# Kernel optimization log

Hardware: AMD Instinct MI355X
Metric: run time of the kernel (lower is better)

## Reference

```python
import jax, jax.numpy as jnp
import numpy as np

EPS = 1e-6
GROUPS = 32


def group_norm(x, scale, bias):
    # x: [b, c, d, h, w]
    b, c, d, h, w = x.shape
    xg = x.reshape(b, GROUPS, c // GROUPS, d, h, w)
    mean = xg.mean(axis=(2, 3, 4, 5), keepdims=True)
    var = xg.var(axis=(2, 3, 4, 5), keepdims=True)
    xn = ((xg - mean) * jax.lax.rsqrt(var + EPS)).reshape(b, c, d, h, w)
    return xn * scale[None, :, None, None, None] + bias[None, :, None, None, None]


def setup_inputs() -> dict:
    key = jax.random.key(0)
    ks = jax.random.split(key, 6)
    C = 512
    x = jax.random.normal(ks[0], (2, C, 16, 16, 16), dtype=jnp.float32)
    s = 1.0 / np.sqrt(C)
    return {
        "x": x,
        "gn_scale": jnp.ones((C,), jnp.float32),
        "gn_bias": jnp.zeros((C,), jnp.float32),
        "wq": jax.random.normal(ks[1], (C, C), jnp.float32) * s,
        "bq": jnp.zeros((C,), jnp.float32),
        "wk": jax.random.normal(ks[2], (C, C), jnp.float32) * s,
        "bk": jnp.zeros((C,), jnp.float32),
        "wv": jax.random.normal(ks[3], (C, C), jnp.float32) * s,
        "bv": jnp.zeros((C,), jnp.float32),
        "wproj": jax.random.normal(ks[4], (C, C), jnp.float32) * s,
        "bproj": jnp.zeros((C,), jnp.float32),
    }


def reference(x, gn_scale, gn_bias, wq, bq, wk, bk, wv, bv, wproj, bproj):
    b, c, d, h, w = x.shape
    h_ = group_norm(x, gn_scale, gn_bias)
    hf = h_.reshape(b, c, d * h * w)  # [b, c, N]
    # 1x1x1 convs == per-position channel matmuls
    q = jnp.einsum("oc,bcn->bon", wq, hf) + bq[None, :, None]
    k = jnp.einsum("oc,bcn->bon", wk, hf) + bk[None, :, None]
    v = jnp.einsum("oc,bcn->bon", wv, hf) + bv[None, :, None]
    # attn[b, i, j] = softmax_j(q_i . k_j / sqrt(c))
    attn = jnp.einsum("bci,bcj->bij", q, k) * (c ** -0.5)
    attn = jax.nn.softmax(attn, axis=-1)
    # out[b, c, i] = sum_j v[b, c, j] * attn[b, i, j]
    out = jnp.einsum("bcj,bij->bci", v, attn)
    out = jnp.einsum("oc,bcn->bon", wproj, out) + bproj[None, :, None]
    return x + out.reshape(b, c, d, h, w)
```

## Files before the change

### kernel.cpp

```cpp
#include <hip/hip_runtime.h>
#include <hip/hip_bf16.h>

#define BB 2
#define CC 512
#define GG 32
#define NN 4096
#define EPSV 1e-6f

typedef __attribute__((ext_vector_type(4))) float f32x4;
typedef __attribute__((ext_vector_type(8))) short s16x8;
typedef __attribute__((ext_vector_type(4))) short s16x4;

__device__ __forceinline__ ushort f2bf(float f){
  union { float f; unsigned u; } v; v.f = f;
  unsigned r = v.u + 0x7fffu + ((v.u >> 16) & 1u);
  return (ushort)(r >> 16);
}
__device__ __forceinline__ short f2bfs(float f){ return (short)f2bf(f); }
__device__ __forceinline__ float b2f(ushort u){
  union { unsigned u; float f; } v; v.u = ((unsigned)u) << 16; return v.f;
}

__device__ __forceinline__ f32x4 mfma16(s16x8 a, s16x8 b, f32x4 c){
  return __builtin_amdgcn_mfma_f32_16x16x32_bf16(a, b, c, 0, 0, 0);
}

#define GLOAD_LDS16(g, l) __builtin_amdgcn_global_load_lds( \
    (const __attribute__((address_space(1))) void*)(g),     \
    (__attribute__((address_space(3))) void*)(l), 16, 0, 0)

__global__ __launch_bounds__(256) void k_convert_w(const float* __restrict__ wq, const float* __restrict__ wk,
                                                   const float* __restrict__ wv, const float* __restrict__ wp,
                                                   ushort* __restrict__ wbf){
  int idx = blockIdx.x * 256 + threadIdx.x;
  const float* srcs[4] = {wq, wk, wv, wp};
  #pragma unroll
  for (int m = 0; m < 4; m++){
    float4 v = reinterpret_cast<const float4*>(srcs[m])[idx];
    ushort4 o; o.x = f2bf(v.x); o.y = f2bf(v.y); o.z = f2bf(v.z); o.w = f2bf(v.w);
    reinterpret_cast<ushort4*>(wbf + (size_t)m * CC * CC)[idx] = o;
  }
}

__global__ __launch_bounds__(256) void k_gn_stats(const float* __restrict__ x, float* __restrict__ stats){
  int bg = blockIdx.x;
  const float* p = x + (size_t)bg * (16 * NN);
  float s = 0.f, ss = 0.f;
  for (int i = threadIdx.x; i < 16 * NN / 4; i += 256){
    float4 v = reinterpret_cast<const float4*>(p)[i];
    s  += v.x + v.y + v.z + v.w;
    ss += v.x*v.x + v.y*v.y + v.z*v.z + v.w*v.w;
  }
  #pragma unroll
  for (int off = 32; off; off >>= 1){ s += __shfl_down(s, off); ss += __shfl_down(ss, off); }
  __shared__ float rs_[4], rss_[4];
  int w = threadIdx.x >> 6, lane = threadIdx.x & 63;
  if (lane == 0){ rs_[w] = s; rss_[w] = ss; }
  __syncthreads();
  if (threadIdx.x == 0){
    float S = rs_[0] + rs_[1] + rs_[2] + rs_[3];
    float SS = rss_[0] + rss_[1] + rss_[2] + rss_[3];
    float inv = 1.0f / (16.0f * NN);
    float mean = S * inv;
    float var = SS * inv - mean * mean;
    stats[bg * 2 + 0] = mean;
    stats[bg * 2 + 1] = rsqrtf(var + EPSV);
  }
}

__global__ __launch_bounds__(256) void k_gn_apply(const float* __restrict__ x, const float* __restrict__ gsc,
                                                  const float* __restrict__ gbi, const float* __restrict__ stats,
                                                  ushort* __restrict__ hf){
  __shared__ ushort tr[32][520];
  int b = blockIdx.y;
  int nb = blockIdx.x * 32;
  int t = threadIdx.x;
  int n = t & 31, cr = t >> 5;
  const float* xb = x + (size_t)b * CC * NN;
  for (int c0 = 0; c0 < CC; c0 += 8){
    int c = c0 + cr;
    float mean = stats[(b * GG + (c >> 4)) * 2 + 0];
    float rstd = stats[(b * GG + (c >> 4)) * 2 + 1];
    float v = xb[(size_t)c * NN + nb + n];
    tr[n][c] = f2bf((v - mean) * rstd * gsc[c] + gbi[c]);
  }
  __syncthreads();
  ushort* out = hf + ((size_t)b * NN + nb) * CC;
  int c8 = (t & 63) * 8;
  int nrow0 = t >> 6;
  #pragma unroll
  for (int i = 0; i < 8; i++){
    int nr = nrow0 + i * 4;
    *reinterpret_cast<s16x8*>(&out[(size_t)nr * CC + c8]) =
      *reinterpret_cast<const s16x8*>(&tr[nr][c8]);
  }
}

__global__ __launch_bounds__(256) void k_gemm_qkv(const ushort* __restrict__ W, const ushort* __restrict__ Bt,
                                                  const float* __restrict__ bq, const float* __restrict__ bk,
                                                  const float* __restrict__ bv,
                                                  ushort* __restrict__ qo, ushort* __restrict__ ko,
                                                  ushort* __restrict__ vo, float rs){
  __shared__ ushort Al[3][64][72];
  __shared__ ushort Bl[64][72];
  __shared__ float bl[3][64];
  int b = blockIdx.z, ob = blockIdx.y * 64, nb = blockIdx.x * 64;
  int t = threadIdx.x, w = t >> 6, l = t & 63;
  int lr = l & 15, lk = l >> 4;
  int wo = (w >> 1) * 32, wn = (w & 1) * 32;
  if (t < 64){ bl[0][t] = bq[ob + t]; bl[1][t] = bk[ob + t]; bl[2][t] = bv[ob + t]; }
  const ushort* Bp = Bt + ((size_t)b * NN + nb) * CC;
  int srow = t >> 2, scol = (t & 3) * 16;
  f32x4 acc[3][2][2] = {};
  for (int k0 = 0; k0 < CC; k0 += 64){
    #pragma unroll
    for (int m = 0; m < 3; m++){
      const ushort* Ap = W + (size_t)m * CC * CC + (size_t)ob * CC;
      *reinterpret_cast<s16x8*>(&Al[m][srow][scol])     = *reinterpret_cast<const s16x8*>(&Ap[(size_t)srow * CC + k0 + scol]);
      *reinterpret_cast<s16x8*>(&Al[m][srow][scol + 8]) = *reinterpret_cast<const s16x8*>(&Ap[(size_t)srow * CC + k0 + scol + 8]);
    }
    *reinterpret_cast<s16x8*>(&Bl[srow][scol])     = *reinterpret_cast<const s16x8*>(&Bp[(size_t)srow * CC + k0 + scol]);
    *reinterpret_cast<s16x8*>(&Bl[srow][scol + 8]) = *reinterpret_cast<const s16x8*>(&Bp[(size_t)srow * CC + k0 + scol + 8]);
    __syncthreads();
    #pragma unroll
    for (int kk = 0; kk < 2; kk++){
      s16x8 b0 = *reinterpret_cast<const s16x8*>(&Bl[wn + lr][kk * 32 + lk * 8]);
      s16x8 b1 = *reinterpret_cast<const s16x8*>(&Bl[wn + 16 + lr][kk * 32 + lk * 8]);
      #pragma unroll
      for (int m = 0; m < 3; m++){
        s16x8 a0 = *reinterpret_cast<const s16x8*>(&Al[m][wo + lr][kk * 32 + lk * 8]);
        s16x8 a1 = *reinterpret_cast<const s16x8*>(&Al[m][wo + 16 + lr][kk * 32 + lk * 8]);
        acc[m][0][0] = mfma16(a0, b0, acc[m][0][0]);
        acc[m][0][1] = mfma16(a0, b1, acc[m][0][1]);
        acc[m][1][0] = mfma16(a1, b0, acc[m][1][0]);
        acc[m][1][1] = mfma16(a1, b1, acc[m][1][1]);
      }
    }
    __syncthreads();
  }
  #pragma unroll
  for (int m = 0; m < 2; m++){
    ushort* dst = (m == 0) ? qo : ko;
    float scl = (m == 0) ? rs : 1.0f;
    #pragma unroll
    for (int oi = 0; oi < 2; oi++)
      #pragma unroll
      for (int nj = 0; nj < 2; nj++){
        int o0 = wo + oi * 16 + lk * 4;
        int n  = nb + wn + nj * 16 + lr;
        s16x4 pv;
        #pragma unroll
        for (int r = 0; r < 4; r++) pv[r] = f2bfs((acc[m][oi][nj][r] + bl[m][o0 + r]) * scl);
        *reinterpret_cast<s16x4*>(&dst[((size_t)b * NN + n) * CC + ob + o0]) = pv;
      }
  }
  #pragma unroll
  for (int oi = 0; oi < 2; oi++)
    #pragma unroll
    for (int nj = 0; nj < 2; nj++){
      int o0 = wo + oi * 16 + lk * 4;
      int ncl = wn + nj * 16 + lr;
      #pragma unroll
      for (int r = 0; r < 4; r++) Al[0][o0 + r][ncl] = f2bf(acc[2][oi][nj][r] + bl[2][o0 + r]);
    }
  __syncthreads();
  {
    int o = t >> 2, ns = (t & 3) * 16;
    ushort* dst = &vo[((size_t)b * CC + ob + o) * NN + nb + ns];
    *reinterpret_cast<s16x8*>(dst)     = *reinterpret_cast<const s16x8*>(&Al[0][o][ns]);
    *reinterpret_cast<s16x8*>(dst + 8) = *reinterpret_cast<const s16x8*>(&Al[0][o][ns + 8]);
  }
}

__global__ __launch_bounds__(256) void k_gemm_s(const ushort* __restrict__ qt, const ushort* __restrict__ kt,
                                                ushort* __restrict__ P, float* __restrict__ part){
  __shared__ __align__(16) char smem[65536];
  int lin = blockIdx.x + 32 * blockIdx.y + 1024 * blockIdx.z;
  int tt0 = (lin & 7) * 256 + (lin >> 3);
  int jblk = tt0 & 31;
  int pair = tt0 >> 5;
  int b = pair >> 5;
  int j0 = jblk * 128, i0 = (pair & 31) * 128;
  int t = threadIdx.x, w = t >> 6, l = t & 63;
  int lr = l & 15, lk = l >> 4;
  int wj = (w >> 1) * 64, wi = (w & 1) * 64;
  const ushort* kb = kt + ((size_t)b * NN + j0) * CC;
  const ushort* qb = qt + ((size_t)b * NN + i0) * CC;
  int srow = l >> 3;
  int schunk = (l & 7) ^ srow;

#define STAGE_S(BUF, K0)                                                          \
  {                                                                               \
    ushort* Ks_ = (ushort*)(smem + (BUF) * 16384);                                \
    ushort* Qs_ = (ushort*)(smem + 32768 + (BUF) * 16384);                        \
    _Pragma("unroll")                                                             \
    for (int tt = 0; tt < 8; tt++){                                               \
      int inst = w * 8 + tt;                                                      \
      if (inst < 16){                                                             \
        const ushort* src = kb + (size_t)(inst * 8 + srow) * CC + (K0) + schunk * 8; \
        GLOAD_LDS16(src, Ks_ + inst * 512);                                       \
      } else {                                                                    \
        int q = inst - 16;                                                        \
        const ushort* src = qb + (size_t)(q * 8 + srow) * CC + (K0) + schunk * 8; \
        GLOAD_LDS16(src, Qs_ + q * 512);                                          \
      }                                                                           \
    }                                                                             \
  }

  f32x4 acc[4][4] = {};
  STAGE_S(0, 0)
  __syncthreads();
  for (int s8 = 0; s8 < 8; s8++){
    if (s8 < 7) STAGE_S((s8 + 1) & 1, (s8 + 1) * 64)
    const ushort* Ks = (const ushort*)(smem + (s8 & 1) * 16384);
    const ushort* Qs = (const ushort*)(smem + 32768 + (s8 & 1) * 16384);
    #pragma unroll
    for (int kk = 0; kk < 2; kk++){
      int xs = ((kk * 4 + lk) ^ (lr & 7)) * 8;
      s16x8 af[4], bf[4];
      #pragma unroll
      for (int s = 0; s < 4; s++){
        af[s] = *(const s16x8*)&Ks[(wj + s * 16 + lr) * 64 + xs];
        bf[s] = *(const s16x8*)&Qs[(wi + s * 16 + lr) * 64 + xs];
      }
      #pragma unroll
      for (int sj = 0; sj < 4; sj++)
        #pragma unroll
        for (int si = 0; si < 4; si++)
          acc[sj][si] = mfma16(af[sj], bf[si], acc[sj][si]);
    }
    __syncthreads();
  }
#undef STAGE_S
  ushort* Pe = (ushort*)smem;
  float rsum[4] = {0.f, 0.f, 0.f, 0.f};
  #pragma unroll
  for (int sj = 0; sj < 4; sj++)
    #pragma unroll
    for (int si = 0; si < 4; si++){
      int il = wi + si * 16 + lr;
      int jl = wj + sj * 16 + lk * 4;
      s16x4 pk;
      #pragma unroll
      for (int r = 0; r < 4; r++){
        float e = exp2f(acc[sj][si][r]);
        pk[r] = f2bfs(e);
        rsum[si] += e;
      }
      *(s16x4*)&Pe[il * 136 + jl] = pk;
    }
  #pragma unroll
  for (int si = 0; si < 4; si++){
    float s = rsum[si];
    s += __shfl_xor(s, 16);
    s += __shfl_xor(s, 32);
    if (lk == 0){
      int il = wi + si * 16 + lr;
      part[((size_t)b * NN + i0 + il) * 64 + jblk * 2 + (w >> 1)] = s;
    }
  }
  __syncthreads();
  {
    int row = t >> 1, cs = (t & 1) * 64;
    ushort* dst = P + ((size_t)b * NN + i0 + row) * NN + j0 + cs;
    #pragma unroll
    for (int k = 0; k < 8; k++)
      *(s16x8*)&dst[k * 8] = *(const s16x8*)&Pe[row * 136 + cs + k * 8];
  }
}

__global__ __launch_bounds__(256) void k_rowsum2(const float* __restrict__ part, float* __restrict__ linv){
  int row = blockIdx.x * 4 + (threadIdx.x >> 6);
  int l = threadIdx.x & 63;
  float s = part[(size_t)row * 64 + l];
  #pragma unroll
  for (int off = 32; off; off >>= 1) s += __shfl_down(s, off);
  if (l == 0) linv[row] = 1.0f / s;
}

__global__ __launch_bounds__(512) void k_gemm_o(const ushort* __restrict__ P, const ushort* __restrict__ vv,
                                                const float* __restrict__ linv, ushort* __restrict__ ot){
  __shared__ __align__(16) char smem[49152];
  int lin = blockIdx.x + 8 * blockIdx.y + 256 * blockIdx.z;
  int tt0 = (lin & 7) * 64 + (lin >> 3);
  int cblk = tt0 & 7;
  int pair = tt0 >> 3;
  int b = pair >> 5;
  int c0 = cblk * 64, i0 = (pair & 31) * 128;
  int t = threadIdx.x, w = t >> 6, l = t & 63;
  int lr = l & 15, lk = l >> 4;
  int wi = (w >> 1) * 32, wc = (w & 1) * 32;
  const ushort* vb = vv + ((size_t)b * CC + c0) * NN;
  const ushort* pb = P + ((size_t)b * NN + i0) * NN;
  int srow = l >> 3;
  int schunk = (l & 7) ^ srow;

#define STAGE_O(BUF, K0)                                                          \
  {                                                                               \
    ushort* Vs_ = (ushort*)(smem + (BUF) * 8192);                                 \
    ushort* Ps_ = (ushort*)(smem + 16384 + (BUF) * 16384);                        \
    _Pragma("unroll")                                                             \
    for (int tt = 0; tt < 3; tt++){                                               \
      int inst = w * 3 + tt;                                                      \
      if (inst < 8){                                                              \
        const ushort* src = vb + (size_t)(inst * 8 + srow) * NN + (K0) + schunk * 8; \
        GLOAD_LDS16(src, Vs_ + inst * 512);                                       \
      } else {                                                                    \
        int q = inst - 8;                                                         \
        const ushort* src = pb + (size_t)(q * 8 + srow) * NN + (K0) + schunk * 8; \
        GLOAD_LDS16(src, Ps_ + q * 512);                                          \
      }                                                                           \
    }                                                                             \
  }

  f32x4 acc[2][2] = {};
  STAGE_O(0, 0)
  __syncthreads();
  for (int s64 = 0; s64 < 64; s64++){
    if (s64 < 63) STAGE_O((s64 + 1) & 1, (s64 + 1) * 64)
    const ushort* Vs = (const ushort*)(smem + (s64 & 1) * 8192);
    const ushort* Ps = (const ushort*)(smem + 16384 + (s64 & 1) * 16384);
    #pragma unroll
    for (int kk = 0; kk < 2; kk++){
      int xs = ((kk * 4 + lk) ^ (lr & 7)) * 8;
      s16x8 af[2], bf[2];
      af[0] = *(const s16x8*)&Vs[(wc + lr) * 64 + xs];
      af[1] = *(const s16x8*)&Vs[(wc + 16 + lr) * 64 + xs];
      bf[0] = *(const s16x8*)&Ps[(wi + lr) * 64 + xs];
      bf[1] = *(const s16x8*)&Ps[(wi + 16 + lr) * 64 + xs];
      acc[0][0] = mfma16(af[0], bf[0], acc[0][0]);
      acc[0][1] = mfma16(af[0], bf[1], acc[0][1]);
      acc[1][0] = mfma16(af[1], bf[0], acc[1][0]);
      acc[1][1] = mfma16(af[1], bf[1], acc[1][1]);
    }
    __syncthreads();
  }
#undef STAGE_O
  ushort* Oe = (ushort*)smem;
  #pragma unroll
  for (int si = 0; si < 2; si++){
    int il = wi + si * 16 + lr;
    float li = linv[(size_t)b * NN + i0 + il];
    #pragma unroll
    for (int sc = 0; sc < 2; sc++){
      int cl = wc + sc * 16 + lk * 4;
      s16x4 pk;
      #pragma unroll
      for (int r = 0; r < 4; r++) pk[r] = f2bfs(acc[sc][si][r] * li);
      *(s16x4*)&Oe[il * 72 + cl] = pk;
    }
  }
  __syncthreads();
  {
    int row = t >> 2, cs = (t & 3) * 16;
    ushort* dst = ot + ((size_t)b * NN + i0 + row) * CC + c0 + cs;
    #pragma unroll
    for (int k = 0; k < 2; k++)
      *(s16x8*)&dst[k * 8] = *(const s16x8*)&Oe[row * 72 + cs + k * 8];
  }
}

__global__ __launch_bounds__(256) void k_gemm_proj(const ushort* __restrict__ A, const ushort* __restrict__ Bt,
                                                   const float* __restrict__ bias, float* __restrict__ o32,
                                                   const float* __restrict__ xres){
  __shared__ ushort Al[64][72];
  __shared__ ushort Bl[64][72];
  __shared__ float bl[64];
  __shared__ float trf[64 * 68];
  int b = blockIdx.z, ob = blockIdx.y * 64, nb = blockIdx.x * 64;
  int t = threadIdx.x, w = t >> 6, l = t & 63;
  int lr = l & 15, lk = l >> 4;
  int wo = (w >> 1) * 32, wn = (w & 1) * 32;
  if (t < 64) bl[t] = bias[ob + t];
  const ushort* Bp = Bt + ((size_t)b * NN + nb) * CC;
  const ushort* Ap = A + (size_t)ob * CC;
  int srow = t >> 2, scol = (t & 3) * 16;
  f32x4 acc[2][2] = {};
  for (int k0 = 0; k0 < CC; k0 += 64){
    *reinterpret_cast<s16x8*>(&Al[srow][scol])     = *reinterpret_cast<const s16x8*>(&Ap[(size_t)srow * CC + k0 + scol]);
    *reinterpret_cast<s16x8*>(&Al[srow][scol + 8]) = *reinterpret_cast<const s16x8*>(&Ap[(size_t)srow * CC + k0 + scol + 8]);
    *reinterpret_cast<s16x8*>(&Bl[srow][scol])     = *reinterpret_cast<const s16x8*>(&Bp[(size_t)srow * CC + k0 + scol]);
    *reinterpret_cast<s16x8*>(&Bl[srow][scol + 8]) = *reinterpret_cast<const s16x8*>(&Bp[(size_t)srow * CC + k0 + scol + 8]);
    __syncthreads();
    #pragma unroll
    for (int kk = 0; kk < 2; kk++){
      s16x8 a0 = *reinterpret_cast<const s16x8*>(&Al[wo + lr][kk * 32 + lk * 8]);
      s16x8 a1 = *reinterpret_cast<const s16x8*>(&Al[wo + 16 + lr][kk * 32 + lk * 8]);
      s16x8 b0 = *reinterpret_cast<const s16x8*>(&Bl[wn + lr][kk * 32 + lk * 8]);
      s16x8 b1 = *reinterpret_cast<const s16x8*>(&Bl[wn + 16 + lr][kk * 32 + lk * 8]);
      acc[0][0] = mfma16(a0, b0, acc[0][0]);
      acc[0][1] = mfma16(a0, b1, acc[0][1]);
      acc[1][0] = mfma16(a1, b0, acc[1][0]);
      acc[1][1] = mfma16(a1, b1, acc[1][1]);
    }
    __syncthreads();
  }
  #pragma unroll
  for (int oi = 0; oi < 2; oi++)
    #pragma unroll
    for (int nj = 0; nj < 2; nj++){
      int o0 = wo + oi * 16 + lk * 4;
      int ncl = wn + nj * 16 + lr;
      #pragma unroll
      for (int r = 0; r < 4; r++) trf[(o0 + r) * 68 + ncl] = acc[oi][nj][r] + bl[o0 + r];
    }
  __syncthreads();
  {
    int o = t >> 2, ns = (t & 3) * 16;
    size_t base = ((size_t)b * CC + ob + o) * NN + nb + ns;
    #pragma unroll
    for (int q = 0; q < 4; q++){
      float4 xv = *reinterpret_cast<const float4*>(&xres[base + q * 4]);
      float4 ov;
      ov.x = xv.x + trf[o * 68 + ns + q * 4 + 0];
      ov.y = xv.y + trf[o * 68 + ns + q * 4 + 1];
      ov.z = xv.z + trf[o * 68 + ns + q * 4 + 2];
      ov.w = xv.w + trf[o * 68 + ns + q * 4 + 3];
      *reinterpret_cast<float4*>(&o32[base + q * 4]) = ov;
    }
  }
}

extern "C" void kernel_launch(void* const* d_in, const int* in_sizes, int n_in,
                              void* d_out, int out_size, void* d_ws, size_t ws_size,
                              hipStream_t stream){
  const float* x   = (const float*)d_in[0];
  const float* gsc = (const float*)d_in[1];
  const float* gbi = (const float*)d_in[2];
  const float* wq  = (const float*)d_in[3];
  const float* bq  = (const float*)d_in[4];
  const float* wk  = (const float*)d_in[5];
  const float* bk  = (const float*)d_in[6];
  const float* wv  = (const float*)d_in[7];
  const float* bv  = (const float*)d_in[8];
  const float* wp  = (const float*)d_in[9];
  const float* bp  = (const float*)d_in[10];
  char* ws = (char*)d_ws;
  const size_t MB = 1024 * 1024;
  ushort* wbf  = (ushort*)ws;
  ushort* qtb  = (ushort*)(ws + 2 * MB);
  ushort* ktb  = (ushort*)(ws + 10 * MB);
  ushort* vvb  = (ushort*)(ws + 18 * MB);
  ushort* hfb  = (ushort*)(ws + 26 * MB);
  ushort* Pbuf = (ushort*)(ws + 34 * MB);
  float* linv  = (float*)(ws + 98 * MB);
  float* stats = (float*)(ws + 98 * MB + 64 * 1024);
  float* part  = (float*)(ws + 26 * MB);
  ushort* otb = hfb;

  const float rs = 0.044194173824159216f * 1.4426950408889634f;

  k_convert_w<<<256, 256, 0, stream>>>(wq, wk, wv, wp, wbf);
  k_gn_stats<<<64, 256, 0, stream>>>(x, stats);
  k_gn_apply<<<dim3(128, 2, 1), 256, 0, stream>>>(x, gsc, gbi, stats, hfb);
  k_gemm_qkv<<<dim3(64, 8, 2), 256, 0, stream>>>(wbf, hfb, bq, bk, bv, qtb, ktb, vvb, rs);
  k_gemm_s<<<dim3(32, 32, 2), 256, 0, stream>>>(qtb, ktb, Pbuf, part);
  k_rowsum2<<<2048, 256, 0, stream>>>(part, linv);
  k_gemm_o<<<dim3(8, 32, 2), 512, 0, stream>>>(Pbuf, vvb, linv, otb);
  k_gemm_proj<<<dim3(64, 8, 2), 256, 0, stream>>>(wbf + 3 * CC * CC, otb, bp, (float*)d_out, x);
}
```

Measured before the change: 194.0 us.

## Double-buffer QKV/proj GEMMs with async LDS loads and shrink S-GEMM k-step

```diff
diff --git a/kernel.cpp b/kernel.cpp
--- a/kernel.cpp
+++ b/kernel.cpp
@@ -96,85 +96,106 @@
   }
 }
 
-__global__ __launch_bounds__(256) void k_gemm_qkv(const ushort* __restrict__ W, const ushort* __restrict__ Bt,
-                                                  const float* __restrict__ bq, const float* __restrict__ bk,
-                                                  const float* __restrict__ bv,
-                                                  ushort* __restrict__ qo, ushort* __restrict__ ko,
-                                                  ushort* __restrict__ vo, float rs){
-  __shared__ ushort Al[3][64][72];
-  __shared__ ushort Bl[64][72];
+__global__ __launch_bounds__(256, 3) void k_gemm_qkv2(const ushort* __restrict__ W, const ushort* __restrict__ Bt,
+                                                      const float* __restrict__ bq, const float* __restrict__ bk,
+                                                      const float* __restrict__ bv,
+                                                      ushort* __restrict__ qo, ushort* __restrict__ ko,
+                                                      ushort* __restrict__ vo, float rs){
+  __shared__ __align__(16) char smem[40960];
   __shared__ float bl[3][64];
-  int b = blockIdx.z, ob = blockIdx.y * 64, nb = blockIdx.x * 64;
+  int b = blockIdx.z, ob = blockIdx.y * 64, nb = blockIdx.x * 128;
   int t = threadIdx.x, w = t >> 6, l = t & 63;
   int lr = l & 15, lk = l >> 4;
-  int wo = (w >> 1) * 32, wn = (w & 1) * 32;
+  int wo = (w >> 1) * 32, wn = (w & 1) * 64;
   if (t < 64){ bl[0][t] = bq[ob + t]; bl[1][t] = bk[ob + t]; bl[2][t] = bv[ob + t]; }
   const ushort* Bp = Bt + ((size_t)b * NN + nb) * CC;
-  int srow = t >> 2, scol = (t & 3) * 16;
-  f32x4 acc[3][2][2] = {};
-  for (int k0 = 0; k0 < CC; k0 += 64){
+  const ushort* Wp = W + (size_t)ob * CC;
+  int srow = l >> 2;
+  int schunk = (l & 3) ^ ((l >> 2) & 3) ^ ((l >> 4) & 3);
+  int xs = (lk ^ (lr & 3) ^ ((lr >> 2) & 3)) * 8;
+
+#define STAGE_QKV(BUF, K0)                                                               \
+  {                                                                                      \
+    ushort* As_ = (ushort*)(smem + (BUF) * 20480);                                       \
+    ushort* Bs_ = As_ + 6144;                                                            \
+    _Pragma("unroll")                                                                    \
+    for (int tt = 0; tt < 5; tt++){                                                      \
+      int inst = w * 5 + tt;                                                             \
+      if (inst < 12){                                                                    \
+        int m = inst >> 2, sub = inst & 3;                                               \
+        const ushort* src = Wp + (size_t)m * CC * CC + (size_t)(sub * 16 + srow) * CC + (K0) + schunk * 8; \
+        GLOAD_LDS16(src, As_ + m * 2048 + sub * 512);                                    \
+      } else {                                                                           \
+        int q = inst - 12;                                                               \
+        const ushort* src = Bp + (size_t)(q * 16 + srow) * CC + (K0) + schunk * 8;       \
+        GLOAD_LDS16(src, Bs_ + q * 512);                                                 \
+      }                                                                                  \
+    }                                                                                    \
+  }
+
+  f32x4 acc[3][2][4] = {};
+  STAGE_QKV(0, 0)
+  __syncthreads();
+  for (int s16 = 0; s16 < 16; s16++){
+    if (s16 < 15) STAGE_QKV((s16 + 1) & 1, (s16 + 1) * 32)
+    const ushort* As = (const ushort*)(smem + (s16 & 1) * 20480);
+    const ushort* Bs = As + 6144;
+    s16x8 bf[4];
+    #pragma unroll
+    for (int sn = 0; sn < 4; sn++)
+      bf[sn] = *(const s16x8*)&Bs[(wn + sn * 16 + lr) * 32 + xs];
     #pragma unroll
     for (int m = 0; m < 3; m++){
-      const ushort* Ap = W + (size_t)m * CC * CC + (size_t)ob * CC;
-      *reinterpret_cast<s16x8*>(&Al[m][srow][scol])     = *reinterpret_cast<const s16x8*>(&Ap[(size_t)srow * CC + k0 + scol]);
-      *reinterpret_cast<s16x8*>(&Al[m][srow][scol + 8]) = *reinterpret_cast<const s16x8*>(&Ap[(size_t)srow * CC + k0 + scol + 8]);
-    }
-    *reinterpret_cast<s16x8*>(&Bl[srow][scol])     = *reinterpret_cast<const s16x8*>(&Bp[(size_t)srow * CC + k0 + scol]);
-    *reinterpret_cast<s16x8*>(&Bl[srow][scol + 8]) = *reinterpret_cast<const s16x8*>(&Bp[(size_t)srow * CC + k0 + scol + 8]);
+      s16x8 a0 = *(const s16x8*)&As[m * 2048 + (wo + lr) * 32 + xs];
+      s16x8 a1 = *(const s16x8*)&As[m * 2048 + (wo + 16 + lr) * 32 + xs];
+      #pragma unroll
+      for (int sn = 0; sn < 4; sn++){
+        acc[m][0][sn] = mfma16(a0, bf[sn], acc[m][0][sn]);
+        acc[m][1][sn] = mfma16(a1, bf[sn], acc[m][1][sn]);
+      }
+    }
     __syncthreads();
-    #pragma unroll
-    for (int kk = 0; kk < 2; kk++){
-      s16x8 b0 = *reinterpret_cast<const s16x8*>(&Bl[wn + lr][kk * 32 + lk * 8]);
-      s16x8 b1 = *reinterpret_cast<const s16x8*>(&Bl[wn + 16 + lr][kk * 32 + lk * 8]);
-      #pragma unroll
-      for (int m = 0; m < 3; m++){
-        s16x8 a0 = *reinterpret_cast<const s16x8*>(&Al[m][wo + lr][kk * 32 + lk * 8]);
-        s16x8 a1 = *reinterpret_cast<const s16x8*>(&Al[m][wo + 16 + lr][kk * 32 + lk * 8]);
-        acc[m][0][0] = mfma16(a0, b0, acc[m][0][0]);
-        acc[m][0][1] = mfma16(a0, b1, acc[m][0][1]);
-        acc[m][1][0] = mfma16(a1, b0, acc[m][1][0]);
-        acc[m][1][1] = mfma16(a1, b1, acc[m][1][1]);
-      }
-    }
-    __syncthreads();
-  }
+  }
+#undef STAGE_QKV
   #pragma unroll
   for (int m = 0; m < 2; m++){
     ushort* dst = (m == 0) ? qo : ko;
     float scl = (m == 0) ? rs : 1.0f;
     #pragma unroll
-    for (int oi = 0; oi < 2; oi++)
-      #pragma unroll
-      for (int nj = 0; nj < 2; nj++){
-        int o0 = wo + oi * 16 + lk * 4;
-        int n  = nb + wn + nj * 16 + lr;
+    for (int so = 0; so < 2; so++)
+      #pragma unroll
+      for (int sn = 0; sn < 4; sn++){
+        int o0 = wo + so * 16 + lk * 4;
+        int n  = nb + wn + sn * 16 + lr;
         s16x4 pv;
         #pragma unroll
-        for (int r = 0; r < 4; r++) pv[r] = f2bfs((acc[m][oi][nj][r] + bl[m][o0 + r]) * scl);
+        for (int r = 0; r < 4; r++) pv[r] = f2bfs((acc[m][so][sn][r] + bl[m][o0 + r]) * scl);
         *reinterpret_cast<s16x4*>(&dst[((size_t)b * NN + n) * CC + ob + o0]) = pv;
       }
   }
-  #pragma unroll
-  for (int oi = 0; oi < 2; oi++)
-    #pragma unroll
-    for (int nj = 0; nj < 2; nj++){
-      int o0 = wo + oi * 16 + lk * 4;
-      int ncl = wn + nj * 16 + lr;
-      #pragma unroll
-      for (int r = 0; r < 4; r++) Al[0][o0 + r][ncl] = f2bf(acc[2][oi][nj][r] + bl[2][o0 + r]);
+  ushort* Ve = (ushort*)smem;
+  #pragma unroll
+  for (int so = 0; so < 2; so++)
+    #pragma unroll
+    for (int sn = 0; sn < 4; sn++){
+      int o0 = wo + so * 16 + lk * 4;
+      int ncl = wn + sn * 16 + lr;
+      #pragma unroll
+      for (int r = 0; r < 4; r++) Ve[(o0 + r) * 136 + ncl] = f2bf(acc[2][so][sn][r] + bl[2][o0 + r]);
     }
   __syncthreads();
   {
-    int o = t >> 2, ns = (t & 3) * 16;
-    ushort* dst = &vo[((size_t)b * CC + ob + o) * NN + nb + ns];
-    *reinterpret_cast<s16x8*>(dst)     = *reinterpret_cast<const s16x8*>(&Al[0][o][ns]);
-    *reinterpret_cast<s16x8*>(dst + 8) = *reinterpret_cast<const s16x8*>(&Al[0][o][ns + 8]);
-  }
-}
-
-__global__ __launch_bounds__(256) void k_gemm_s(const ushort* __restrict__ qt, const ushort* __restrict__ kt,
-                                                ushort* __restrict__ P, float* __restrict__ part){
-  __shared__ __align__(16) char smem[65536];
+    int row = t >> 2, cs = (t & 3) * 32;
+    ushort* dst = &vo[((size_t)b * CC + ob + row) * NN + nb + cs];
+    #pragma unroll
+    for (int k = 0; k < 4; k++)
+      *(s16x8*)&dst[k * 8] = *(const s16x8*)&Ve[row * 136 + cs + k * 8];
+  }
+}
+
+__global__ __launch_bounds__(256, 4) void k_gemm_s(const ushort* __restrict__ qt, const ushort* __restrict__ kt,
+                                                   ushort* __restrict__ P, float* __restrict__ part){
+  __shared__ __align__(16) char smem[35840];
   int lin = blockIdx.x + 32 * blockIdx.y + 1024 * blockIdx.z;
   int tt0 = (lin & 7) * 256 + (lin >> 3);
   int jblk = tt0 & 31;
@@ -186,22 +207,23 @@
   int wj = (w >> 1) * 64, wi = (w & 1) * 64;
   const ushort* kb = kt + ((size_t)b * NN + j0) * CC;
   const ushort* qb = qt + ((size_t)b * NN + i0) * CC;
-  int srow = l >> 3;
-  int schunk = (l & 7) ^ srow;
+  int srow = l >> 2;
+  int schunk = (l & 3) ^ ((l >> 2) & 3) ^ ((l >> 4) & 3);
+  int xs = (lk ^ (lr & 3) ^ ((lr >> 2) & 3)) * 8;
 
 #define STAGE_S(BUF, K0)                                                          \
   {                                                                               \
-    ushort* Ks_ = (ushort*)(smem + (BUF) * 16384);                                \
-    ushort* Qs_ = (ushort*)(smem + 32768 + (BUF) * 16384);                        \
+    ushort* Ks_ = (ushort*)(smem + (BUF) * 8192);                                 \
+    ushort* Qs_ = (ushort*)(smem + 16384 + (BUF) * 8192);                         \
     _Pragma("unroll")                                                             \
-    for (int tt = 0; tt < 8; tt++){                                               \
-      int inst = w * 8 + tt;                                                      \
-      if (inst < 16){                                                             \
-        const ushort* src = kb + (size_t)(inst * 8 + srow) * CC + (K0) + schunk * 8; \
+    for (int tt = 0; tt < 4; tt++){                                               \
+      int inst = w * 4 + tt;                                                      \
+      if (inst < 8){                                                              \
+        const ushort* src = kb + (size_t)(inst * 16 + srow) * CC + (K0) + schunk * 8; \
         GLOAD_LDS16(src, Ks_ + inst * 512);                                       \
       } else {                                                                    \
-        int q = inst - 16;                                                        \
-        const ushort* src = qb + (size_t)(q * 8 + srow) * CC + (K0) + schunk * 8; \
+        int q = inst - 8;                                                         \
+        const ushort* src = qb + (size_t)(q * 16 + srow) * CC + (K0) + schunk * 8; \
         GLOAD_LDS16(src, Qs_ + q * 512);                                          \
       }                                                                           \
     }                                                                             \
@@ -210,25 +232,21 @@
   f32x4 acc[4][4] = {};
   STAGE_S(0, 0)
   __syncthreads();
-  for (int s8 = 0; s8 < 8; s8++){
-    if (s8 < 7) STAGE_S((s8 + 1) & 1, (s8 + 1) * 64)
-    const ushort* Ks = (const ushort*)(smem + (s8 & 1) * 16384);
-    const ushort* Qs = (const ushort*)(smem + 32768 + (s8 & 1) * 16384);
-    #pragma unroll
-    for (int kk = 0; kk < 2; kk++){
-      int xs = ((kk * 4 + lk) ^ (lr & 7)) * 8;
-      s16x8 af[4], bf[4];
-      #pragma unroll
-      for (int s = 0; s < 4; s++){
-        af[s] = *(const s16x8*)&Ks[(wj + s * 16 + lr) * 64 + xs];
-        bf[s] = *(const s16x8*)&Qs[(wi + s * 16 + lr) * 64 + xs];
-      }
-      #pragma unroll
-      for (int sj = 0; sj < 4; sj++)
-        #pragma unroll
-        for (int si = 0; si < 4; si++)
-          acc[sj][si] = mfma16(af[sj], bf[si], acc[sj][si]);
-    }
+  for (int s8 = 0; s8 < 16; s8++){
+    if (s8 < 15) STAGE_S((s8 + 1) & 1, (s8 + 1) * 32)
+    const ushort* Ks = (const ushort*)(smem + (s8 & 1) * 8192);
+    const ushort* Qs = (const ushort*)(smem + 16384 + (s8 & 1) * 8192);
+    s16x8 af[4], bf[4];
+    #pragma unroll
+    for (int s = 0; s < 4; s++){
+      af[s] = *(const s16x8*)&Ks[(wj + s * 16 + lr) * 32 + xs];
+      bf[s] = *(const s16x8*)&Qs[(wi + s * 16 + lr) * 32 + xs];
+    }
+    #pragma unroll
+    for (int sj = 0; sj < 4; sj++)
+      #pragma unroll
+      for (int si = 0; si < 4; si++)
+        acc[sj][si] = mfma16(af[sj], bf[si], acc[sj][si]);
     __syncthreads();
   }
 #undef STAGE_S
@@ -360,62 +378,80 @@
   }
 }
 
-__global__ __launch_bounds__(256) void k_gemm_proj(const ushort* __restrict__ A, const ushort* __restrict__ Bt,
-                                                   const float* __restrict__ bias, float* __restrict__ o32,
-                                                   const float* __restrict__ xres){
-  __shared__ ushort Al[64][72];
-  __shared__ ushort Bl[64][72];
+__global__ __launch_bounds__(256, 3) void k_gemm_proj2(const ushort* __restrict__ A, const ushort* __restrict__ Bt,
+                                                       const float* __restrict__ bias, float* __restrict__ o32,
+                                                       const float* __restrict__ xres){
+  __shared__ __align__(16) char smem[34048];
   __shared__ float bl[64];
-  __shared__ float trf[64 * 68];
-  int b = blockIdx.z, ob = blockIdx.y * 64, nb = blockIdx.x * 64;
+  int b = blockIdx.z, ob = blockIdx.y * 64, nb = blockIdx.x * 128;
   int t = threadIdx.x, w = t >> 6, l = t & 63;
   int lr = l & 15, lk = l >> 4;
-  int wo = (w >> 1) * 32, wn = (w & 1) * 32;
+  int wo = (w >> 1) * 32, wn = (w & 1) * 64;
   if (t < 64) bl[t] = bias[ob + t];
   const ushort* Bp = Bt + ((size_t)b * NN + nb) * CC;
   const ushort* Ap = A + (size_t)ob * CC;
-  int srow = t >> 2, scol = (t & 3) * 16;
-  f32x4 acc[2][2] = {};
-  for (int k0 = 0; k0 < CC; k0 += 64){
-    *reinterpret_cast<s16x8*>(&Al[srow][scol])     = *reinterpret_cast<const s16x8*>(&Ap[(size_t)srow * CC + k0 + scol]);
-    *reinterpret_cast<s16x8*>(&Al[srow][scol + 8]) = *reinterpret_cast<const s16x8*>(&Ap[(size_t)srow * CC + k0 + scol + 8]);
-    *reinterpret_cast<s16x8*>(&Bl[srow][scol])     = *reinterpret_cast<const s16x8*>(&Bp[(size_t)srow * CC + k0 + scol]);
-    *reinterpret_cast<s16x8*>(&Bl[srow][scol + 8]) = *reinterpret_cast<const s16x8*>(&Bp[(size_t)srow * CC + k0 + scol + 8]);
+  int srow = l >> 2;
+  int schunk = (l & 3) ^ ((l >> 2) & 3) ^ ((l >> 4) & 3);
+  int xs = (lk ^ (lr & 3) ^ ((lr >> 2) & 3)) * 8;
+
+#define STAGE_P2(BUF, K0)                                                         \
+  {                                                                               \
+    ushort* As_ = (ushort*)(smem + (BUF) * 12288);                                \
+    ushort* Bs_ = As_ + 2048;                                                     \
+    _Pragma("unroll")                                                             \
+    for (int tt = 0; tt < 3; tt++){                                               \
+      int inst = w * 3 + tt;                                                      \
+      if (inst < 4){                                                              \
+        const ushort* src = Ap + (size_t)(inst * 16 + srow) * CC + (K0) + schunk * 8; \
+        GLOAD_LDS16(src, As_ + inst * 512);                                       \
+      } else {                                                                    \
+        int q = inst - 4;                                                         \
+        const ushort* src = Bp + (size_t)(q * 16 + srow) * CC + (K0) + schunk * 8; \
+        GLOAD_LDS16(src, Bs_ + q * 512);                                          \
+      }                                                                           \
+    }                                                                             \
+  }
+
+  f32x4 acc[2][4] = {};
+  STAGE_P2(0, 0)
+  __syncthreads();
+  for (int s16 = 0; s16 < 16; s16++){
+    if (s16 < 15) STAGE_P2((s16 + 1) & 1, (s16 + 1) * 32)
+    const ushort* As = (const ushort*)(smem + (s16 & 1) * 12288);
+    const ushort* Bs = As + 2048;
+    s16x8 a0 = *(const s16x8*)&As[(wo + lr) * 32 + xs];
+    s16x8 a1 = *(const s16x8*)&As[(wo + 16 + lr) * 32 + xs];
+    #pragma unroll
+    for (int sn = 0; sn < 4; sn++){
+      s16x8 bf = *(const s16x8*)&Bs[(wn + sn * 16 + lr) * 32 + xs];
+      acc[0][sn] = mfma16(a0, bf, acc[0][sn]);
+      acc[1][sn] = mfma16(a1, bf, acc[1][sn]);
+    }
     __syncthreads();
-    #pragma unroll
-    for (int kk = 0; kk < 2; kk++){
-      s16x8 a0 = *reinterpret_cast<const s16x8*>(&Al[wo + lr][kk * 32 + lk * 8]);
-      s16x8 a1 = *reinterpret_cast<const s16x8*>(&Al[wo + 16 + lr][kk * 32 + lk * 8]);
-      s16x8 b0 = *reinterpret_cast<const s16x8*>(&Bl[wn + lr][kk * 32 + lk * 8]);
-      s16x8 b1 = *reinterpret_cast<const s16x8*>(&Bl[wn + 16 + lr][kk * 32 + lk * 8]);
-      acc[0][0] = mfma16(a0, b0, acc[0][0]);
-      acc[0][1] = mfma16(a0, b1, acc[0][1]);
-      acc[1][0] = mfma16(a1, b0, acc[1][0]);
-      acc[1][1] = mfma16(a1, b1, acc[1][1]);
-    }
-    __syncthreads();
-  }
-  #pragma unroll
-  for (int oi = 0; oi < 2; oi++)
-    #pragma unroll
-    for (int nj = 0; nj < 2; nj++){
-      int o0 = wo + oi * 16 + lk * 4;
-      int ncl = wn + nj * 16 + lr;
-      #pragma unroll
-      for (int r = 0; r < 4; r++) trf[(o0 + r) * 68 + ncl] = acc[oi][nj][r] + bl[o0 + r];
+  }
+#undef STAGE_P2
+  float* trf = (float*)smem;
+  #pragma unroll
+  for (int so = 0; so < 2; so++)
+    #pragma unroll
+    for (int sn = 0; sn < 4; sn++){
+      int o0 = wo + so * 16 + lk * 4;
+      int ncl = wn + sn * 16 + lr;
+      #pragma unroll
+      for (int r = 0; r < 4; r++) trf[(o0 + r) * 133 + ncl] = acc[so][sn][r] + bl[o0 + r];
     }
   __syncthreads();
   {
-    int o = t >> 2, ns = (t & 3) * 16;
-    size_t base = ((size_t)b * CC + ob + o) * NN + nb + ns;
-    #pragma unroll
-    for (int q = 0; q < 4; q++){
+    int row = t >> 2, cs = (t & 3) * 32;
+    size_t base = ((size_t)b * CC + ob + row) * NN + nb + cs;
+    #pragma unroll
+    for (int q = 0; q < 8; q++){
       float4 xv = *reinterpret_cast<const float4*>(&xres[base + q * 4]);
       float4 ov;
-      ov.x = xv.x + trf[o * 68 + ns + q * 4 + 0];
-      ov.y = xv.y + trf[o * 68 + ns + q * 4 + 1];
-      ov.z = xv.z + trf[o * 68 + ns + q * 4 + 2];
-      ov.w = xv.w + trf[o * 68 + ns + q * 4 + 3];
+      ov.x = xv.x + trf[row * 133 + cs + q * 4 + 0];
+      ov.y = xv.y + trf[row * 133 + cs + q * 4 + 1];
+      ov.z = xv.z + trf[row * 133 + cs + q * 4 + 2];
+      ov.w = xv.w + trf[row * 133 + cs + q * 4 + 3];
       *reinterpret_cast<float4*>(&o32[base + q * 4]) = ov;
     }
   }
@@ -453,9 +489,9 @@
   k_convert_w<<<256, 256, 0, stream>>>(wq, wk, wv, wp, wbf);
   k_gn_stats<<<64, 256, 0, stream>>>(x, stats);
   k_gn_apply<<<dim3(128, 2, 1), 256, 0, stream>>>(x, gsc, gbi, stats, hfb);
-  k_gemm_qkv<<<dim3(64, 8, 2), 256, 0, stream>>>(wbf, hfb, bq, bk, bv, qtb, ktb, vvb, rs);
+  k_gemm_qkv2<<<dim3(32, 8, 2), 256, 0, stream>>>(wbf, hfb, bq, bk, bv, qtb, ktb, vvb, rs);
   k_gemm_s<<<dim3(32, 32, 2), 256, 0, stream>>>(qtb, ktb, Pbuf, part);
   k_rowsum2<<<2048, 256, 0, stream>>>(part, linv);
   k_gemm_o<<<dim3(8, 32, 2), 512, 0, stream>>>(Pbuf, vvb, linv, otb);
-  k_gemm_proj<<<dim3(64, 8, 2), 256, 0, stream>>>(wbf + 3 * CC * CC, otb, bp, (float*)d_out, x);
-}
+  k_gemm_proj2<<<dim3(32, 8, 2), 256, 0, stream>>>(wbf + 3 * CC * CC, otb, bp, (float*)d_out, x);
+}
```

Measured after the change: 204.5 us. +5.4%, slower.
